# Kernel tuning notes

Hardware: AMD Instinct MI355X
Metric: run time of the kernel (lower is better)

Reference implementation:

```python
import jax, jax.numpy as jnp
import numpy as np
import math

D_MODEL = 1024
NUM_HEADS = 16
D_K = D_MODEL // NUM_HEADS
THETA = 10000.0
B, T = 2, 2048


def _trunc_normal(key, shape, std):
    # truncated normal in [-3std, 3std]
    return jax.random.truncated_normal(key, -3.0, 3.0, shape, jnp.float32) * std


def setup_inputs() -> dict:
    key = jax.random.key(0)
    ks = jax.random.split(key, 6)
    sigma = math.sqrt(2.0 / (D_MODEL + D_MODEL))
    x = jax.random.normal(ks[0], (B, T, D_MODEL), jnp.float32)
    Wq = _trunc_normal(ks[1], (D_MODEL, D_MODEL), sigma)  # [out, in]
    Wk = _trunc_normal(ks[2], (D_MODEL, D_MODEL), sigma)
    Wv = _trunc_normal(ks[3], (D_MODEL, D_MODEL), sigma)
    Wo = _trunc_normal(ks[4], (D_MODEL, D_MODEL), sigma)
    token_positions = jnp.arange(T, dtype=jnp.int64 if jax.config.read('jax_enable_x64') else jnp.int32)
    return {"x": x, "Wq": Wq, "Wk": Wk, "Wv": Wv, "Wo": Wo,
            "token_positions": token_positions}


def _rotate_half(x):
    x0 = x[..., ::2]
    x1 = x[..., 1::2]
    return jnp.stack((-x1, x0), axis=-1).reshape(x.shape)


def _rope(x, token_positions):
    # x: [B, H, T, d_k]; token_positions: [T]
    inv_freq = 1.0 / (THETA ** (jnp.arange(0, D_K, 2, dtype=jnp.float32) / D_K))
    ang = token_positions.astype(jnp.float32)[:, None] * inv_freq  # [T, d_k/2]
    cos = jnp.repeat(jnp.cos(ang), 2, axis=-1)  # [T, d_k]
    sin = jnp.repeat(jnp.sin(ang), 2, axis=-1)
    xdtype = x.dtype
    xf = x.astype(jnp.float32)
    return (xf * cos + _rotate_half(xf) * sin).astype(xdtype)


def reference(x, Wq, Wk, Wv, Wo, token_positions):
    b, t, _ = x.shape

    def proj_split(W):
        h = jnp.einsum('btd,od->bto', x, W)
        return h.reshape(b, t, NUM_HEADS, D_K).transpose(0, 2, 1, 3)  # [B,H,T,d_k]

    Q = _rope(proj_split(Wq), token_positions)
    K = _rope(proj_split(Wk), token_positions)
    V = proj_split(Wv)

    scores = jnp.einsum('bhqd,bhkd->bhqk', Q, K) / math.sqrt(D_K)
    causal = jnp.tril(jnp.ones((t, t), dtype=bool))  # [T,T]
    scores = jnp.where(causal, scores, -jnp.inf)
    weights = jax.nn.softmax(scores, axis=-1)
    attn = jnp.einsum('bhqk,bhkd->bhqd', weights, V)  # [B,H,T,d_v]
    merged = attn.transpose(0, 2, 1, 3).reshape(b, t, D_MODEL)
    return jnp.einsum('btd,od->bto', merged, Wo)
```

## Files before the change

kernel.cpp:

```cpp
#include <hip/hip_runtime.h>
#include <cstdint>
#include <cstddef>

#define DMODEL 1024
#define NHEADS 16
#define DKH    64
#define SEQT   2048
#define NBATCH 2
#define MTOT   (NBATCH*SEQT)

#define QSCALE 0.1803368801111204f

using h16   = _Float16;
using h16x2 = __attribute__((ext_vector_type(2))) h16;
using h16x4 = __attribute__((ext_vector_type(4))) h16;
using h16x8 = __attribute__((ext_vector_type(8))) h16;
using f32x4 = __attribute__((ext_vector_type(4))) float;
using fp16x2_native = __attribute__((ext_vector_type(2))) __fp16;

using as1_void = __attribute__((address_space(1))) void;
using as3_void = __attribute__((address_space(3))) void;

__device__ __forceinline__ void gll16(void* lds, const void* g) {
  __builtin_amdgcn_global_load_lds((const as1_void*)g, (as3_void*)lds, 16, 0, 0);
}

__device__ __forceinline__ h16x2 pkrtz(float a, float b) {
  fp16x2_native t = __builtin_amdgcn_cvt_pkrtz(a, b);
  h16x2 r; r[0] = (h16)t[0]; r[1] = (h16)t[1]; return r;
}

__device__ __forceinline__ h16x4 cvt4(const float4 v) {
  h16x4 o; o[0] = (h16)v.x; o[1] = (h16)v.y; o[2] = (h16)v.z; o[3] = (h16)v.w; return o;
}

__global__ void prep_kernel(const float4* __restrict__ x,
                            const float4* __restrict__ Wq, const float4* __restrict__ Wk,
                            const float4* __restrict__ Wv, const float4* __restrict__ Wo,
                            h16x4* __restrict__ xb,
                            h16x4* __restrict__ wqb, h16x4* __restrict__ wkb,
                            h16x4* __restrict__ wvb, h16x4* __restrict__ wob,
                            float* __restrict__ ctab, float* __restrict__ stab) {
  const int tid  = blockIdx.x * blockDim.x + threadIdx.x;
  const int nthr = gridDim.x * blockDim.x;
  const int NX4 = MTOT * DMODEL / 4;
  const int NW4 = DMODEL * DMODEL / 4;
  for (int i = tid; i < NX4; i += nthr) xb[i] = cvt4(x[i]);
  for (int i = tid; i < NW4; i += nthr) {
    wqb[i] = cvt4(Wq[i]);
    wkb[i] = cvt4(Wk[i]);
    wvb[i] = cvt4(Wv[i]);
    wob[i] = cvt4(Wo[i]);
  }
  for (int i = tid; i < SEQT * 32; i += nthr) {
    const int t = i >> 5, fi = i & 31;
    float inv = __expf(-0.28782313662425575f * (float)fi);
    float ang = (float)t * inv;
    float s, c;
    sincosf(ang, &s, &c);
    ctab[i] = c; stab[i] = s;
  }
}

__device__ __forceinline__ void gemm128_bt(const h16* __restrict__ A, const h16* __restrict__ Bt,
                                           int m0, int n0, h16* Al, h16* Bl, f32x4 acc[4][4]) {
  const int tid  = threadIdx.x;
  const int lane = tid & 63;
  const int wv   = tid >> 6;
  const int wm = (wv >> 1) * 64, wn = (wv & 1) * 64;
  const int lr = lane & 15, lk = (lane >> 4) * 8;
  const int srow = tid >> 2, scol = (tid & 3) * 8;
  const h16* a0 = A  + (size_t)(m0 + srow) * DMODEL + scol;
  const h16* a1 = a0 + (size_t)64 * DMODEL;
  const h16* b0 = Bt + (size_t)(n0 + srow) * DMODEL + scol;
  const h16* b1 = b0 + (size_t)64 * DMODEL;
  h16* alds0 = Al + wv * 512;
  h16* alds1 = Al + 2048 + wv * 512;
  h16* blds0 = Bl + wv * 512;
  h16* blds1 = Bl + 2048 + wv * 512;

  for (int k0 = 0; k0 < DMODEL; k0 += 32) {
    __syncthreads();
    gll16(alds0, a0 + k0);
    gll16(alds1, a1 + k0);
    gll16(blds0, b0 + k0);
    gll16(blds1, b1 + k0);
    __syncthreads();
    h16x8 af[4], bfr[4];
#pragma unroll
    for (int i = 0; i < 4; ++i) {
      af[i]  = *(const h16x8*)(Al + (wm + i * 16 + lr) * 32 + lk);
      bfr[i] = *(const h16x8*)(Bl + (wn + i * 16 + lr) * 32 + lk);
    }
#pragma unroll
    for (int i = 0; i < 4; ++i)
#pragma unroll
      for (int j = 0; j < 4; ++j)
        acc[i][j] = __builtin_amdgcn_mfma_f32_16x16x32_f16(af[i], bfr[j], acc[i][j], 0, 0, 0);
  }
}

__global__ __launch_bounds__(256, 2) void qkv_kernel(
    const h16* __restrict__ xb,
    const h16* __restrict__ wqb, const h16* __restrict__ wkb, const h16* __restrict__ wvb,
    const float* __restrict__ ctab, const float* __restrict__ stab,
    h16* __restrict__ Qb, h16* __restrict__ Kb, h16* __restrict__ Vt) {
  __shared__ h16 Al[128 * 32], Bl[128 * 32];
  const int which = blockIdx.z;
  const h16* W = (which == 0) ? wqb : (which == 1) ? wkb : wvb;
  const int m0 = blockIdx.x * 128, n0 = blockIdx.y * 128;
  f32x4 acc[4][4];
  const f32x4 zero4 = {0.f, 0.f, 0.f, 0.f};
#pragma unroll
  for (int i = 0; i < 4; ++i)
#pragma unroll
    for (int j = 0; j < 4; ++j) acc[i][j] = zero4;

  gemm128_bt(xb, W, m0, n0, Al, Bl, acc);

  const int lane = threadIdx.x & 63, wv = threadIdx.x >> 6;
  const int wm = (wv >> 1) * 64, wn = (wv & 1) * 64;
  const int lr4 = ((lane >> 4) << 2), lc = lane & 15;
  if (which == 2) {
#pragma unroll
    for (int i = 0; i < 4; ++i) {
      const int m = m0 + wm + i * 16 + lr4;
      const int b = m >> 11, t = m & (SEQT - 1);
#pragma unroll
      for (int j = 0; j < 4; ++j) {
        const int n = n0 + wn + j * 16 + lc;
        const int h = n >> 6, d = n & 63;
        h16x4 o4;
#pragma unroll
        for (int r = 0; r < 4; ++r) o4[r] = (h16)acc[i][j][r];
        *(h16x4*)&Vt[((size_t)(b * NHEADS + h) * DKH + d) * SEQT + t] = o4;
      }
    }
  } else {
#pragma unroll
    for (int i = 0; i < 4; ++i) {
#pragma unroll
      for (int j = 0; j < 4; ++j) {
        const int n = n0 + wn + j * 16 + lc;
        const int h = n >> 6, d = n & 63;
#pragma unroll
        for (int r = 0; r < 4; ++r) {
          const int m = m0 + wm + i * 16 + lr4 + r;
          const int b = m >> 11, t = m & (SEQT - 1);
          float v = acc[i][j][r];
          float pv = __shfl_xor(v, 1);
          const int fi = d >> 1;
          float c = ctab[t * 32 + fi], s = stab[t * 32 + fi];
          float res = (d & 1) ? (v * c + pv * s) : (v * c - pv * s);
          if (which == 0) res *= QSCALE;
          h16* dst = (which == 0) ? Qb : Kb;
          dst[((size_t)(b * NHEADS + h) * SEQT + t) * DKH + d] = (h16)res;
        }
      }
    }
  }
}

__global__ __launch_bounds__(256, 4) void attn_kernel(
    const h16* __restrict__ Qb, const h16* __restrict__ Kb,
    const h16* __restrict__ Vt, h16* __restrict__ Mg) {
  __shared__ h16 Kl[128][76];
  __shared__ h16 Vl[64][140];
  const int i = blockIdx.x;
  const int qt = (i & 1) ? (31 - (i >> 1)) : (i >> 1);
  const int bh = blockIdx.y;
  const int b = bh >> 4, h = bh & 15;
  const int tid = threadIdx.x, lane = tid & 63, wv = tid >> 6;
  const int lr = lane & 15, lg = lane >> 4;
  const int q0 = qt * 64;
  const int qbase = q0 + wv * 16;
  const int q = qbase + lr;
  const h16* Qp = Qb + ((size_t)bh * SEQT + qbase) * DKH;
  const h16* Kp = Kb + (size_t)bh * SEQT * DKH;
  const h16* Vp = Vt + (size_t)bh * DKH * SEQT;

  h16x8 qf[2];
#pragma unroll
  for (int kk = 0; kk < 2; ++kk)
    qf[kk] = *(const h16x8*)(Qp + lr * DKH + kk * 32 + lg * 8);

  float mrow = -3.0e38f, lsum = 0.f;
  f32x4 o[4];
  const f32x4 zero4 = {0.f, 0.f, 0.f, 0.f};
#pragma unroll
  for (int di = 0; di < 4; ++di) o[di] = zero4;

  const int sr = tid >> 2, sc = (tid & 3) * 16;
  const int nkt = (qt >> 1) + 1;
  for (int kt = 0; kt < nkt; ++kt) {
    const int k0 = kt * 128;
    __syncthreads();
#pragma unroll
    for (int half = 0; half < 2; ++half) {
      const int r = half * 64 + sr;
      *(uint4*)&Kl[r][sc]     = *(const uint4*)(Kp + (size_t)(k0 + r) * DKH + sc);
      *(uint4*)&Kl[r][sc + 8] = *(const uint4*)(Kp + (size_t)(k0 + r) * DKH + sc + 8);
    }
#pragma unroll
    for (int half = 0; half < 2; ++half) {
      const int c = half * 64 + sc;
      *(uint4*)&Vl[sr][c]     = *(const uint4*)(Vp + (size_t)sr * SEQT + k0 + c);
      *(uint4*)&Vl[sr][c + 8] = *(const uint4*)(Vp + (size_t)sr * SEQT + k0 + c + 8);
    }
    __syncthreads();

    f32x4 s[8];
    __builtin_amdgcn_s_setprio(1);
#pragma unroll
    for (int ni = 0; ni < 8; ++ni) {
      s[ni] = zero4;
#pragma unroll
      for (int kk = 0; kk < 2; ++kk) {
        h16x8 kf = *(const h16x8*)&Kl[ni * 16 + lr][kk * 32 + lg * 8];
        s[ni] = __builtin_amdgcn_mfma_f32_16x16x32_f16(kf, qf[kk], s[ni], 0, 0, 0);
      }
    }
    __builtin_amdgcn_s_setprio(0);

    if (kt == nkt - 1) {
#pragma unroll
      for (int ni = 0; ni < 8; ++ni)
#pragma unroll
        for (int r = 0; r < 4; ++r) {
          const int key = k0 + ni * 16 + lg * 4 + r;
          if (key > q) s[ni][r] = -3.0e38f;
        }
    }

    float mx = s[0][0];
#pragma unroll
    for (int ni = 0; ni < 8; ++ni)
#pragma unroll
      for (int r = 0; r < 4; ++r) mx = fmaxf(mx, s[ni][r]);
    mx = fmaxf(mx, __shfl_xor(mx, 16));
    mx = fmaxf(mx, __shfl_xor(mx, 32));
    if (mx > mrow + 11.0f) {
      const float mnew = fmaxf(mrow, mx);
      const float scl = exp2f(mrow - mnew);
      mrow = mnew;
      lsum *= scl;
#pragma unroll
      for (int di = 0; di < 4; ++di)
#pragma unroll
        for (int r = 0; r < 4; ++r) o[di][r] *= scl;
    }
    float rs = 0.f;
#pragma unroll
    for (int ni = 0; ni < 8; ++ni)
#pragma unroll
      for (int r = 0; r < 4; ++r) {
        float p = exp2f(s[ni][r] - mrow);
        s[ni][r] = p;
        rs += p;
      }
    rs += __shfl_xor(rs, 16);
    rs += __shfl_xor(rs, 32);
    lsum += rs;

    __builtin_amdgcn_s_setprio(1);
#pragma unroll
    for (int ni = 0; ni < 8; ++ni) {
      h16x2 plo = pkrtz(s[ni][0], s[ni][1]);
      h16x2 phi = pkrtz(s[ni][2], s[ni][3]);
      h16x4 pb; pb[0] = plo[0]; pb[1] = plo[1]; pb[2] = phi[0]; pb[3] = phi[1];
#pragma unroll
      for (int di = 0; di < 4; ++di) {
        h16x4 va = *(const h16x4*)&Vl[di * 16 + lr][ni * 16 + lg * 4];
        o[di] = __builtin_amdgcn_mfma_f32_16x16x16f16(va, pb, o[di], 0, 0, 0);
      }
    }
    __builtin_amdgcn_s_setprio(0);
  }

  __syncthreads();
  const float inv = 1.0f / lsum;
#pragma unroll
  for (int di = 0; di < 4; ++di) {
    h16x2 lo = pkrtz(o[di][0] * inv, o[di][1] * inv);
    h16x2 hi = pkrtz(o[di][2] * inv, o[di][3] * inv);
    h16x4 o4; o4[0] = lo[0]; o4[1] = lo[1]; o4[2] = hi[0]; o4[3] = hi[1];
    *(h16x4*)&Kl[wv * 16 + lr][di * 16 + lg * 4] = o4;
  }
  __syncthreads();
  {
    const int row = tid >> 2, c0 = (tid & 3) * 16;
    h16* dst = Mg + ((size_t)(b * SEQT + q0 + row)) * DMODEL + h * DKH + c0;
    *(uint4*)dst       = *(const uint4*)&Kl[row][c0];
    *(uint4*)(dst + 8) = *(const uint4*)&Kl[row][c0 + 8];
  }
}

__global__ __launch_bounds__(256, 2) void proj_kernel(
    const h16* __restrict__ Mg, const h16* __restrict__ wob, float* __restrict__ out) {
  __shared__ h16 Al[128 * 32], Bl[128 * 32];
  const int m0 = blockIdx.x * 128, n0 = blockIdx.y * 128;
  f32x4 acc[4][4];
  const f32x4 zero4 = {0.f, 0.f, 0.f, 0.f};
#pragma unroll
  for (int i = 0; i < 4; ++i)
#pragma unroll
    for (int j = 0; j < 4; ++j) acc[i][j] = zero4;

  gemm128_bt(Mg, wob, m0, n0, Al, Bl, acc);

  const int lane = threadIdx.x & 63, wv = threadIdx.x >> 6;
  const int wm = (wv >> 1) * 64, wn = (wv & 1) * 64;
  const int lr4 = ((lane >> 4) << 2), lc = lane & 15;
#pragma unroll
  for (int i = 0; i < 4; ++i)
#pragma unroll
    for (int j = 0; j < 4; ++j) {
      const int n = n0 + wn + j * 16 + lc;
#pragma unroll
      for (int r = 0; r < 4; ++r) {
        const int m = m0 + wm + i * 16 + lr4 + r;
        out[(size_t)m * DMODEL + n] = acc[i][j][r];
      }
    }
}

extern "C" void kernel_launch(void* const* d_in, const int* in_sizes, int n_in,
                              void* d_out, int out_size, void* d_ws, size_t ws_size,
                              hipStream_t stream) {
  (void)in_sizes; (void)n_in; (void)out_size; (void)ws_size;
  const float* x  = (const float*)d_in[0];
  const float* Wq = (const float*)d_in[1];
  const float* Wk = (const float*)d_in[2];
  const float* Wv = (const float*)d_in[3];
  const float* Wo = (const float*)d_in[4];
  float* out = (float*)d_out;

  char* w = (char*)d_ws;
  h16* xb  = (h16*)w; w += (size_t)MTOT * DMODEL * 2;
  h16* wqb = (h16*)w; w += (size_t)DMODEL * DMODEL * 2;
  h16* wkb = (h16*)w; w += (size_t)DMODEL * DMODEL * 2;
  h16* wvb = (h16*)w; w += (size_t)DMODEL * DMODEL * 2;
  h16* wob = (h16*)w; w += (size_t)DMODEL * DMODEL * 2;
  h16* Qb  = (h16*)w; w += (size_t)MTOT * DMODEL * 2;
  h16* Kb  = (h16*)w; w += (size_t)MTOT * DMODEL * 2;
  h16* Vt  = (h16*)w; w += (size_t)MTOT * DMODEL * 2;
  h16* Mg  = (h16*)w; w += (size_t)MTOT * DMODEL * 2;
  float* ctab = (float*)w; w += (size_t)SEQT * 32 * 4;
  float* stab = (float*)w; w += (size_t)SEQT * 32 * 4;

  prep_kernel<<<1024, 256, 0, stream>>>((const float4*)x, (const float4*)Wq, (const float4*)Wk,
                                        (const float4*)Wv, (const float4*)Wo,
                                        (h16x4*)xb, (h16x4*)wqb, (h16x4*)wkb, (h16x4*)wvb,
                                        (h16x4*)wob, ctab, stab);
  qkv_kernel<<<dim3(32, 8, 3), 256, 0, stream>>>(xb, wqb, wkb, wvb, ctab, stab, Qb, Kb, Vt);
  attn_kernel<<<dim3(32, 32), 256, 0, stream>>>(Qb, Kb, Vt, Mg);
  proj_kernel<<<dim3(32, 8), 256, 0, stream>>>(Mg, wob, out);
}
```

Measured before the change: 132.4 us.

## Double query tile per attention block to reuse K/V tiles across two sub-tiles

```diff
diff --git a/kernel.cpp b/kernel.cpp
--- a/kernel.cpp
+++ b/kernel.cpp
@@ -166,132 +166,149 @@
     const h16* __restrict__ Vt, h16* __restrict__ Mg) {
   __shared__ h16 Kl[128][76];
   __shared__ h16 Vl[64][140];
-  const int i = blockIdx.x;
-  const int qt = (i & 1) ? (31 - (i >> 1)) : (i >> 1);
-  const int bh = blockIdx.y;
+  const int linear = blockIdx.x + 16 * blockIdx.y;
+  const int v    = linear & 7;
+  const int p    = linear >> 3;
+  const int half = p >> 5;
+  const int bh   = p & 31;
+  const int u    = (half + bh) & 1;
+  const int qt   = u ? (15 - v) : v;
   const int b = bh >> 4, h = bh & 15;
   const int tid = threadIdx.x, lane = tid & 63, wv = tid >> 6;
   const int lr = lane & 15, lg = lane >> 4;
-  const int q0 = qt * 64;
-  const int qbase = q0 + wv * 16;
-  const int q = qbase + lr;
+  const int q0 = qt * 128;
+  const int qbase = q0 + wv * 32;
   const h16* Qp = Qb + ((size_t)bh * SEQT + qbase) * DKH;
   const h16* Kp = Kb + (size_t)bh * SEQT * DKH;
   const h16* Vp = Vt + (size_t)bh * DKH * SEQT;
 
-  h16x8 qf[2];
-#pragma unroll
-  for (int kk = 0; kk < 2; ++kk)
-    qf[kk] = *(const h16x8*)(Qp + lr * DKH + kk * 32 + lg * 8);
-
-  float mrow = -3.0e38f, lsum = 0.f;
-  f32x4 o[4];
+  h16x8 qf[2][2];
+#pragma unroll
+  for (int sub = 0; sub < 2; ++sub)
+#pragma unroll
+    for (int kk = 0; kk < 2; ++kk)
+      qf[sub][kk] = *(const h16x8*)(Qp + (sub * 16 + lr) * DKH + kk * 32 + lg * 8);
+
+  float mrow[2] = {-3.0e38f, -3.0e38f}, lsum[2] = {0.f, 0.f};
+  f32x4 oA[4], oB[4];
   const f32x4 zero4 = {0.f, 0.f, 0.f, 0.f};
 #pragma unroll
-  for (int di = 0; di < 4; ++di) o[di] = zero4;
+  for (int di = 0; di < 4; ++di) { oA[di] = zero4; oB[di] = zero4; }
 
   const int sr = tid >> 2, sc = (tid & 3) * 16;
-  const int nkt = (qt >> 1) + 1;
+  const int nkt = qt + 1;
   for (int kt = 0; kt < nkt; ++kt) {
     const int k0 = kt * 128;
     __syncthreads();
 #pragma unroll
-    for (int half = 0; half < 2; ++half) {
-      const int r = half * 64 + sr;
+    for (int hh = 0; hh < 2; ++hh) {
+      const int r = hh * 64 + sr;
       *(uint4*)&Kl[r][sc]     = *(const uint4*)(Kp + (size_t)(k0 + r) * DKH + sc);
       *(uint4*)&Kl[r][sc + 8] = *(const uint4*)(Kp + (size_t)(k0 + r) * DKH + sc + 8);
     }
 #pragma unroll
-    for (int half = 0; half < 2; ++half) {
-      const int c = half * 64 + sc;
+    for (int hh = 0; hh < 2; ++hh) {
+      const int c = hh * 64 + sc;
       *(uint4*)&Vl[sr][c]     = *(const uint4*)(Vp + (size_t)sr * SEQT + k0 + c);
       *(uint4*)&Vl[sr][c + 8] = *(const uint4*)(Vp + (size_t)sr * SEQT + k0 + c + 8);
     }
     __syncthreads();
 
-    f32x4 s[8];
-    __builtin_amdgcn_s_setprio(1);
-#pragma unroll
-    for (int ni = 0; ni < 8; ++ni) {
-      s[ni] = zero4;
-#pragma unroll
-      for (int kk = 0; kk < 2; ++kk) {
-        h16x8 kf = *(const h16x8*)&Kl[ni * 16 + lr][kk * 32 + lg * 8];
-        s[ni] = __builtin_amdgcn_mfma_f32_16x16x32_f16(kf, qf[kk], s[ni], 0, 0, 0);
-      }
-    }
-    __builtin_amdgcn_s_setprio(0);
-
-    if (kt == nkt - 1) {
+    const bool diag = (kt == nkt - 1);
+#pragma unroll
+    for (int sub = 0; sub < 2; ++sub) {
+      const int q = qbase + sub * 16 + lr;
+      f32x4* o = sub ? oB : oA;
+
+      f32x4 s[8];
+      __builtin_amdgcn_s_setprio(1);
+#pragma unroll
+      for (int ni = 0; ni < 8; ++ni) {
+        s[ni] = zero4;
+#pragma unroll
+        for (int kk = 0; kk < 2; ++kk) {
+          h16x8 kf = *(const h16x8*)&Kl[ni * 16 + lr][kk * 32 + lg * 8];
+          s[ni] = __builtin_amdgcn_mfma_f32_16x16x32_f16(kf, qf[sub][kk], s[ni], 0, 0, 0);
+        }
+      }
+      __builtin_amdgcn_s_setprio(0);
+
+      if (diag) {
+#pragma unroll
+        for (int ni = 0; ni < 8; ++ni)
+#pragma unroll
+          for (int r = 0; r < 4; ++r) {
+            const int key = k0 + ni * 16 + lg * 4 + r;
+            if (key > q) s[ni][r] = -3.0e38f;
+          }
+      }
+
+      float mx = s[0][0];
 #pragma unroll
       for (int ni = 0; ni < 8; ++ni)
 #pragma unroll
+        for (int r = 0; r < 4; ++r) mx = fmaxf(mx, s[ni][r]);
+      mx = fmaxf(mx, __shfl_xor(mx, 16));
+      mx = fmaxf(mx, __shfl_xor(mx, 32));
+      if (mx > mrow[sub] + 11.0f) {
+        const float mnew = fmaxf(mrow[sub], mx);
+        const float scl = exp2f(mrow[sub] - mnew);
+        mrow[sub] = mnew;
+        lsum[sub] *= scl;
+#pragma unroll
+        for (int di = 0; di < 4; ++di)
+#pragma unroll
+          for (int r = 0; r < 4; ++r) o[di][r] *= scl;
+      }
+      float rs = 0.f;
+#pragma unroll
+      for (int ni = 0; ni < 8; ++ni)
+#pragma unroll
         for (int r = 0; r < 4; ++r) {
-          const int key = k0 + ni * 16 + lg * 4 + r;
-          if (key > q) s[ni][r] = -3.0e38f;
+          float p2 = exp2f(s[ni][r] - mrow[sub]);
+          s[ni][r] = p2;
+          rs += p2;
         }
-    }
-
-    float mx = s[0][0];
-#pragma unroll
-    for (int ni = 0; ni < 8; ++ni)
-#pragma unroll
-      for (int r = 0; r < 4; ++r) mx = fmaxf(mx, s[ni][r]);
-    mx = fmaxf(mx, __shfl_xor(mx, 16));
-    mx = fmaxf(mx, __shfl_xor(mx, 32));
-    if (mx > mrow + 11.0f) {
-      const float mnew = fmaxf(mrow, mx);
-      const float scl = exp2f(mrow - mnew);
-      mrow = mnew;
-      lsum *= scl;
-#pragma unroll
-      for (int di = 0; di < 4; ++di)
-#pragma unroll
-        for (int r = 0; r < 4; ++r) o[di][r] *= scl;
-    }
-    float rs = 0.f;
-#pragma unroll
-    for (int ni = 0; ni < 8; ++ni)
-#pragma unroll
-      for (int r = 0; r < 4; ++r) {
-        float p = exp2f(s[ni][r] - mrow);
-        s[ni][r] = p;
-        rs += p;
-      }
-    rs += __shfl_xor(rs, 16);
-    rs += __shfl_xor(rs, 32);
-    lsum += rs;
-
-    __builtin_amdgcn_s_setprio(1);
-#pragma unroll
-    for (int ni = 0; ni < 8; ++ni) {
-      h16x2 plo = pkrtz(s[ni][0], s[ni][1]);
-      h16x2 phi = pkrtz(s[ni][2], s[ni][3]);
-      h16x4 pb; pb[0] = plo[0]; pb[1] = plo[1]; pb[2] = phi[0]; pb[3] = phi[1];
-#pragma unroll
-      for (int di = 0; di < 4; ++di) {
-        h16x4 va = *(const h16x4*)&Vl[di * 16 + lr][ni * 16 + lg * 4];
-        o[di] = __builtin_amdgcn_mfma_f32_16x16x16f16(va, pb, o[di], 0, 0, 0);
-      }
-    }
-    __builtin_amdgcn_s_setprio(0);
+      rs += __shfl_xor(rs, 16);
+      rs += __shfl_xor(rs, 32);
+      lsum[sub] += rs;
+
+      __builtin_amdgcn_s_setprio(1);
+#pragma unroll
+      for (int ni = 0; ni < 8; ++ni) {
+        h16x2 plo = pkrtz(s[ni][0], s[ni][1]);
+        h16x2 phi = pkrtz(s[ni][2], s[ni][3]);
+        h16x4 pb; pb[0] = plo[0]; pb[1] = plo[1]; pb[2] = phi[0]; pb[3] = phi[1];
+#pragma unroll
+        for (int di = 0; di < 4; ++di) {
+          h16x4 va = *(const h16x4*)&Vl[di * 16 + lr][ni * 16 + lg * 4];
+          o[di] = __builtin_amdgcn_mfma_f32_16x16x16f16(va, pb, o[di], 0, 0, 0);
+        }
+      }
+      __builtin_amdgcn_s_setprio(0);
+    }
   }
 
   __syncthreads();
-  const float inv = 1.0f / lsum;
-#pragma unroll
-  for (int di = 0; di < 4; ++di) {
-    h16x2 lo = pkrtz(o[di][0] * inv, o[di][1] * inv);
-    h16x2 hi = pkrtz(o[di][2] * inv, o[di][3] * inv);
-    h16x4 o4; o4[0] = lo[0]; o4[1] = lo[1]; o4[2] = hi[0]; o4[3] = hi[1];
-    *(h16x4*)&Kl[wv * 16 + lr][di * 16 + lg * 4] = o4;
+#pragma unroll
+  for (int sub = 0; sub < 2; ++sub) {
+    const float inv = 1.0f / lsum[sub];
+    const f32x4* o = sub ? oB : oA;
+#pragma unroll
+    for (int di = 0; di < 4; ++di) {
+      h16x2 lo = pkrtz(o[di][0] * inv, o[di][1] * inv);
+      h16x2 hi = pkrtz(o[di][2] * inv, o[di][3] * inv);
+      h16x4 o4; o4[0] = lo[0]; o4[1] = lo[1]; o4[2] = hi[0]; o4[3] = hi[1];
+      *(h16x4*)&Kl[wv * 32 + sub * 16 + lr][di * 16 + lg * 4] = o4;
+    }
   }
   __syncthreads();
   {
-    const int row = tid >> 2, c0 = (tid & 3) * 16;
+    const int row = tid >> 1, c0 = (tid & 1) * 32;
     h16* dst = Mg + ((size_t)(b * SEQT + q0 + row)) * DMODEL + h * DKH + c0;
-    *(uint4*)dst       = *(const uint4*)&Kl[row][c0];
-    *(uint4*)(dst + 8) = *(const uint4*)&Kl[row][c0 + 8];
+#pragma unroll
+    for (int uu = 0; uu < 4; ++uu)
+      *(uint4*)(dst + uu * 8) = *(const uint4*)&Kl[row][c0 + uu * 8];
   }
 }
 
@@ -353,6 +370,6 @@
                                         (h16x4*)xb, (h16x4*)wqb, (h16x4*)wkb, (h16x4*)wvb,
                                         (h16x4*)wob, ctab, stab);
   qkv_kernel<<<dim3(32, 8, 3), 256, 0, stream>>>(xb, wqb, wkb, wvb, ctab, stab, Qb, Kb, Vt);
-  attn_kernel<<<dim3(32, 32), 256, 0, stream>>>(Qb, Kb, Vt, Mg);
+  attn_kernel<<<dim3(16, 32), 256, 0, stream>>>(Qb, Kb, Vt, Mg);
   proj_kernel<<<dim3(32, 8), 256, 0, stream>>>(Mg, wob, out);
 }
```

New measurement: 146.7 us. +10.8%, slower.
